# Optimization experiments

Hardware: AMD Instinct MI355X
Metric: run time of the kernel (lower is better)

Reference implementation:

```python
import math
import jax, jax.numpy as jnp
import numpy as np


def _proj(x, w, b):
    # 1x1x1 Conv3d == pointwise channel matmul: (B,C,T,H,W) x (O,C) -> (B,O,T,H,W)
    return jnp.einsum('bcthw,oc->bothw', x, w) + b[None, :, None, None, None]


def setup_inputs() -> dict:
    key = jax.random.key(0)
    ks = jax.random.split(key, 16)
    B, C, T, H, W = 2, 64, 16, 14, 14
    CI = C // 2
    s_in = 1.0 / math.sqrt(C)
    s_out = 1.0 / math.sqrt(CI)
    inp = {'x': jax.random.normal(ks[0], (B, C, T, H, W), jnp.float32)}
    # QKV projections for spatial (s) and temporal (t) branches: (CI, C) weights
    pnames = ['qs', 'ks', 'vs', 'qt', 'kt', 'vt']
    for i, n in enumerate(pnames):
        inp['W' + n] = jax.random.normal(ks[1 + i], (CI, C), jnp.float32) * s_in
        inp['b' + n] = jax.random.normal(ks[7 + i], (CI,), jnp.float32) * 0.01
    # output projection W: (C, CI)
    inp['Ww'] = jax.random.normal(ks[13], (C, CI), jnp.float32) * s_out
    inp['bw'] = jax.random.normal(ks[14], (C,), jnp.float32) * 0.01
    return inp


def reference(x, Wqs, bqs, Wks, bks, Wvs, bvs, Wqt, bqt, Wkt, bkt, Wvt, bvt, Ww, bw):
    B, C, T, H, W = x.shape
    CI = Wqs.shape[0]
    N = CI * H * W  # flat dim after original's raw .view (mixes channel & spatial/time)
    scale = 1.0 / math.sqrt(T)

    # ---- spatial branch: .view(B, T, -1) raw reshape of (B,CI,T,H,W) ----
    qs = _proj(x, Wqs, bqs).reshape(B, T, N).transpose(0, 2, 1)   # (B,N,T)
    ks_ = _proj(x, Wks, bks).reshape(B, T, N)                     # (B,T,N)
    vs = _proj(x, Wvs, bvs).reshape(B, T, N).transpose(0, 2, 1)   # (B,N,T)
    attn_s = jax.nn.softmax(jnp.einsum('bnt,btm->bnm', qs, ks_) * scale, axis=-1)  # (B,N,N)
    ys = jnp.einsum('bnm,bmt->bnt', attn_s, vs)                   # (B,N,T)
    ys = ys.transpose(0, 2, 1).reshape(B, CI, T, H, W)

    # ---- temporal branch: .view(B, CI*H*W, -1) raw reshape ----
    qt = _proj(x, Wqt, bqt).reshape(B, N, T).transpose(0, 2, 1)   # (B,T,N)
    kt = _proj(x, Wkt, bkt).reshape(B, N, T)                      # (B,N,T)
    vt = _proj(x, Wvt, bvt).reshape(B, N, T).transpose(0, 2, 1)   # (B,T,N)
    attn_t = jax.nn.softmax(jnp.einsum('btn,bns->bts', qt, kt) * scale, axis=-1)  # (B,T,T)
    yt = jnp.einsum('bts,bsn->btn', attn_t, vt)                   # (B,T,N)
    yt = yt.transpose(0, 2, 1).reshape(B, CI, T, H, W)

    y = ys + yt
    return _proj(y, Ww, bw) + x
```

## Files before the change

kernel.cpp:

```cpp
#include <hip/hip_runtime.h>
#include <math.h>

#define S3   3136
#define PB   100352
#define XB   200704
#define NN   6272

typedef __attribute__((ext_vector_type(8))) short bf16x8;
typedef __attribute__((ext_vector_type(4))) float f32x4;

__device__ inline ushort f2bf(float f) {
    uint u = __float_as_uint(f);
    return (ushort)((u + 0x7FFFu + ((u >> 16) & 1u)) >> 16);
}

__global__ __launch_bounds__(256) void proj_kernel(
    const float* __restrict__ x,
    const float* __restrict__ W0, const float* __restrict__ b0,
    const float* __restrict__ W1, const float* __restrict__ b1,
    const float* __restrict__ W2, const float* __restrict__ b2,
    const float* __restrict__ W3, const float* __restrict__ b3,
    const float* __restrict__ W4, const float* __restrict__ b4,
    const float* __restrict__ W5, const float* __restrict__ b5,
    ushort* __restrict__ Qb, ushort* __restrict__ Kb, ushort* __restrict__ Vb,
    float* __restrict__ Qt, float* __restrict__ Kt, float* __restrict__ Vt,
    int* __restrict__ cnt)
{
    if (blockIdx.x == 0 && blockIdx.y == 0 && blockIdx.z == 0 && threadIdx.x < 2)
        cnt[threadIdx.x] = 0;

    const float* Wp; const float* bp;
    switch (blockIdx.y) {
        case 0:  Wp = W0; bp = b0; break;
        case 1:  Wp = W1; bp = b1; break;
        case 2:  Wp = W2; bp = b2; break;
        case 3:  Wp = W3; bp = b3; break;
        case 4:  Wp = W4; bp = b4; break;
        default: Wp = W5; bp = b5; break;
    }
    int z = blockIdx.z;

    int gid = blockIdx.x * 256 + threadIdx.x;
    if (gid >= 2 * S3) return;
    int b = (gid >= S3) ? 1 : 0;
    int s = gid - b * S3;

    float xr[64];
    #pragma unroll
    for (int c = 0; c < 64; ++c) xr[c] = x[(size_t)b * XB + (size_t)c * S3 + s];

    float a[16];
    #pragma unroll
    for (int oo = 0; oo < 16; ++oo) {
        int o = z * 16 + oo;
        float acc = bp[o];
        #pragma unroll
        for (int c = 0; c < 64; ++c) acc = fmaf(Wp[o * 64 + c], xr[c], acc);
        a[oo] = acc;
    }

    if (blockIdx.y < 2) {
        const float sc = (blockIdx.y == 0) ? 0.36067376022224085f : 1.0f;
        ushort* ob = (blockIdx.y == 0) ? Qb : Kb;
        #pragma unroll
        for (int h = 0; h < 2; ++h) {
            int n = h * S3 + s;
            uint u0 = f2bf(a[0 + h] * sc)  | ((uint)f2bf(a[2 + h]  * sc) << 16);
            uint u1 = f2bf(a[4 + h] * sc)  | ((uint)f2bf(a[6 + h]  * sc) << 16);
            uint u2 = f2bf(a[8 + h] * sc)  | ((uint)f2bf(a[10 + h] * sc) << 16);
            uint u3 = f2bf(a[12 + h] * sc) | ((uint)f2bf(a[14 + h] * sc) << 16);
            *(uint4*)(ob + ((size_t)(b * NN + n) * 16 + z * 8)) = make_uint4(u0, u1, u2, u3);
        }
    } else if (blockIdx.y == 2) {
        #pragma unroll
        for (int oo = 0; oo < 16; ++oo) {
            int o = z * 16 + oo;
            Vb[(size_t)(b * 16 + (o >> 1)) * NN + (o & 1) * S3 + s] = f2bf(a[oo]);
        }
    } else {
        float* op = (blockIdx.y == 3) ? Qt : (blockIdx.y == 4) ? Kt : Vt;
        #pragma unroll
        for (int oo = 0; oo < 16; ++oo)
            op[(size_t)b * PB + (size_t)(z * 16 + oo) * S3 + s] = a[oo];
    }
}

__global__ __launch_bounds__(256, 4) void attn_kernel(
    const ushort* __restrict__ Qb, const ushort* __restrict__ Kb,
    const ushort* __restrict__ Vb, const float* __restrict__ Qt,
    const float* __restrict__ Kt,
    float* __restrict__ Y, float* __restrict__ Gpart,
    float* __restrict__ At, int* __restrict__ cnt)
{
    __shared__ __align__(16) char smem[16384];
    const int tid = threadIdx.x;
    const int bid = blockIdx.x;

    if (bid < 784) {
        ushort* ptile = (ushort*)smem;
        float*  smY   = (float*)(smem + 5120);
        float*  sml   = (float*)(smem + 9472);

        int wave = __builtin_amdgcn_readfirstlane((int)(tid >> 6));
        int lane = tid & 63;
        int col  = lane & 15;
        int kg   = lane >> 4;
        int b    = (bid >= 392) ? 1 : 0;
        int ntile = bid - b * 392;
        int nbase = ntile * 16;
        int m0    = wave * 1568;

        bf16x8 qf = {0, 0, 0, 0, 0, 0, 0, 0};
        if (kg < 2)
            qf = *(const bf16x8*)(Qb + ((size_t)(b * NN + nbase + col) * 16 + kg * 8));

        const bf16x8 ones = {16256, 16256, 16256, 16256, 16256, 16256, 16256, 16256};
        f32x4 zero4 = {0.f, 0.f, 0.f, 0.f};
        f32x4 yacc  = zero4;
        f32x4 lacc  = zero4;

        ushort* myt = ptile + wave * 640;

        for (int it = 0; it < 49; ++it) {
            int mb = m0 + it * 32;
            bf16x8 vf = *(const bf16x8*)(Vb + ((size_t)(b * 16 + col) * NN + mb + kg * 8));

            #pragma unroll
            for (int tile = 0; tile < 2; ++tile) {
                int mt = mb + tile * 16;
                bf16x8 kf = {0, 0, 0, 0, 0, 0, 0, 0};
                if (kg < 2)
                    kf = *(const bf16x8*)(Kb + ((size_t)(b * NN + mt + col) * 16 + kg * 8));
                f32x4 st = __builtin_amdgcn_mfma_f32_16x16x32_bf16(kf, qf, zero4, 0, 0, 0);
                float p0 = __builtin_amdgcn_exp2f(st[0]);
                float p1 = __builtin_amdgcn_exp2f(st[1]);
                float p2 = __builtin_amdgcn_exp2f(st[2]);
                float p3 = __builtin_amdgcn_exp2f(st[3]);
                uint lo = f2bf(p0) | ((uint)f2bf(p1) << 16);
                uint hi = f2bf(p2) | ((uint)f2bf(p3) << 16);
                *(uint2*)(myt + (col * 40 + tile * 16 + kg * 4)) = make_uint2(lo, hi);
            }
            bf16x8 pf = *(bf16x8*)(myt + (col * 40 + kg * 8));
            yacc = __builtin_amdgcn_mfma_f32_16x16x32_bf16(vf, pf, yacc, 0, 0, 0);
            lacc = __builtin_amdgcn_mfma_f32_16x16x32_bf16(ones, pf, lacc, 0, 0, 0);
        }

        #pragma unroll
        for (int r = 0; r < 4; ++r)
            smY[(wave * 16 + kg * 4 + r) * 17 + col] = yacc[r];
        if (kg == 0) sml[wave * 16 + col] = lacc[0];
        __syncthreads();

        int t  = tid >> 4;
        int nn = tid & 15;
        float a = smY[(0 * 16 + t) * 17 + nn] + smY[(1 * 16 + t) * 17 + nn]
                + smY[(2 * 16 + t) * 17 + nn] + smY[(3 * 16 + t) * 17 + nn];
        float l = sml[0 * 16 + nn] + sml[1 * 16 + nn]
                + sml[2 * 16 + nn] + sml[3 * 16 + nn];
        Y[(size_t)b * PB + (size_t)t * NN + nbase + nn] = a / l;
    } else {
        float* qs = (float*)smem;
        float* ks = qs + 1568;
        int*   flag = (int*)(smem + 16000);

        int gb = bid - 784;
        int b  = gb >> 4;
        int ch = gb & 15;
        int t  = tid >> 4, s2 = tid & 15;

        float acc = 0.0f;
        for (int sub = 0; sub < 4; ++sub) {
            size_t base = (size_t)b * PB + (size_t)(ch * 392 + sub * 98) * 16;
            __syncthreads();
            for (int i = tid; i < 392; i += 256) {
                ((float4*)qs)[i] = ((const float4*)(Qt + base))[i];
                ((float4*)ks)[i] = ((const float4*)(Kt + base))[i];
            }
            __syncthreads();
            #pragma unroll 7
            for (int n = 0; n < 98; ++n)
                acc = fmaf(qs[n * 16 + t], ks[n * 16 + s2], acc);
        }
        Gpart[(size_t)(b * 16 + ch) * 256 + tid] = acc;

        __threadfence();
        __syncthreads();
        if (tid == 0) {
            int old = atomicAdd(cnt + b, 1);
            *flag = (old == 15);
        }
        __syncthreads();
        if (*flag) {
            __threadfence();
            float a = 0.0f;
            #pragma unroll
            for (int c = 0; c < 16; ++c)
                a += Gpart[(size_t)(b * 16 + c) * 256 + tid];
            qs[tid] = a * 0.25f;
            __syncthreads();
            if (tid < 16) {
                const float* Lr = &qs[tid * 16];
                float mx = -1e30f;
                #pragma unroll
                for (int s = 0; s < 16; ++s) mx = fmaxf(mx, Lr[s]);
                float e[16]; float sm = 0.0f;
                #pragma unroll
                for (int s = 0; s < 16; ++s) { e[s] = __expf(Lr[s] - mx); sm += e[s]; }
                float inv = 1.0f / sm;
                #pragma unroll
                for (int s = 0; s < 16; ++s) At[b * 256 + tid * 16 + s] = e[s] * inv;
            }
        }
    }
}

__global__ __launch_bounds__(256) void merge_final(
    const float* __restrict__ Y, const float* __restrict__ At,
    const float* __restrict__ Vt, const float* __restrict__ x,
    const float* __restrict__ Ww, const float* __restrict__ bw,
    float* __restrict__ out)
{
    __shared__ float Ash[16 * 17];
    __shared__ float Wsh[64 * 36];
    __shared__ float Ysh[16 * 36];

    int b  = blockIdx.y;
    int sc = blockIdx.x;
    int tid = threadIdx.x;

    {
        int s2 = tid >> 4, t2 = tid & 15;
        Ash[s2 * 17 + t2] = At[b * 256 + t2 * 16 + s2];
        for (int i = tid; i < 2048; i += 256)
            Wsh[(i >> 5) * 36 + (i & 31)] = Ww[i];
    }
    __syncthreads();

    #pragma unroll
    for (int k = 0; k < 2; ++k) {
        int idx = tid + k * 256;
        int ss = idx & 15;
        int ci = idx >> 4;
        int s  = sc * 16 + ss;
        int t  = ci >> 1;
        int nn = (ci & 1) * S3 + s;

        float ys = Y[(size_t)b * PB + (size_t)ci * S3 + s];

        int t2 = nn & 15;
        const float4* vp = (const float4*)(Vt + (size_t)b * PB + (size_t)t * NN + (nn & ~15));
        float4 v0 = vp[0], v1 = vp[1], v2 = vp[2], v3 = vp[3];
        float yt = Ash[0 * 17 + t2] * v0.x;
        yt = fmaf(Ash[1 * 17 + t2],  v0.y, yt); yt = fmaf(Ash[2 * 17 + t2],  v0.z, yt);
        yt = fmaf(Ash[3 * 17 + t2],  v0.w, yt); yt = fmaf(Ash[4 * 17 + t2],  v1.x, yt);
        yt = fmaf(Ash[5 * 17 + t2],  v1.y, yt); yt = fmaf(Ash[6 * 17 + t2],  v1.z, yt);
        yt = fmaf(Ash[7 * 17 + t2],  v1.w, yt); yt = fmaf(Ash[8 * 17 + t2],  v2.x, yt);
        yt = fmaf(Ash[9 * 17 + t2],  v2.y, yt); yt = fmaf(Ash[10 * 17 + t2], v2.z, yt);
        yt = fmaf(Ash[11 * 17 + t2], v2.w, yt); yt = fmaf(Ash[12 * 17 + t2], v3.x, yt);
        yt = fmaf(Ash[13 * 17 + t2], v3.y, yt); yt = fmaf(Ash[14 * 17 + t2], v3.z, yt);
        yt = fmaf(Ash[15 * 17 + t2], v3.w, yt);

        Ysh[ss * 36 + ci] = ys + yt;
    }
    __syncthreads();

    int ss  = tid & 15;
    int cg4 = tid >> 4;
    int s   = sc * 16 + ss;

    float acc[4];
    #pragma unroll
    for (int k = 0; k < 4; ++k) acc[k] = bw[k * 16 + cg4];

    #pragma unroll
    for (int cb = 0; cb < 32; cb += 4) {
        float4 y4 = *(const float4*)&Ysh[ss * 36 + cb];
        #pragma unroll
        for (int k = 0; k < 4; ++k) {
            float4 w4 = *(const float4*)&Wsh[(k * 16 + cg4) * 36 + cb];
            acc[k] = fmaf(w4.x, y4.x, acc[k]);
            acc[k] = fmaf(w4.y, y4.y, acc[k]);
            acc[k] = fmaf(w4.z, y4.z, acc[k]);
            acc[k] = fmaf(w4.w, y4.w, acc[k]);
        }
    }

    #pragma unroll
    for (int k = 0; k < 4; ++k) {
        int c = k * 16 + cg4;
        size_t o = (size_t)b * XB + (size_t)c * S3 + s;
        out[o] = x[o] + acc[k];
    }
}

extern "C" void kernel_launch(void* const* d_in, const int* in_sizes, int n_in,
                              void* d_out, int out_size, void* d_ws, size_t ws_size,
                              hipStream_t stream)
{
    const float* x   = (const float*)d_in[0];
    const float* Wqs = (const float*)d_in[1];  const float* bqs = (const float*)d_in[2];
    const float* Wks = (const float*)d_in[3];  const float* bks = (const float*)d_in[4];
    const float* Wvs = (const float*)d_in[5];  const float* bvs = (const float*)d_in[6];
    const float* Wqt = (const float*)d_in[7];  const float* bqt = (const float*)d_in[8];
    const float* Wkt = (const float*)d_in[9];  const float* bkt = (const float*)d_in[10];
    const float* Wvt = (const float*)d_in[11]; const float* bvt = (const float*)d_in[12];
    const float* Ww  = (const float*)d_in[13]; const float* bw  = (const float*)d_in[14];

    float* ws = (float*)d_ws;
    int*    cnt = (int*)ws;
    ushort* Qb  = (ushort*)(ws + 4);
    ushort* Kb  = (ushort*)(ws + 100356);
    ushort* Vb  = (ushort*)(ws + 200708);
    float* Qt   = ws + 301060;
    float* Kt   = ws + 501764;
    float* Vt   = ws + 702468;
    float* Y    = ws + 903172;
    float* Gpart = ws + 1103876;
    float* At    = ws + 1112068;

    proj_kernel<<<dim3(25, 6, 2), 256, 0, stream>>>(
        x, Wqs, bqs, Wks, bks, Wvs, bvs, Wqt, bqt, Wkt, bkt, Wvt, bvt,
        Qb, Kb, Vb, Qt, Kt, Vt, cnt);

    attn_kernel<<<816, 256, 0, stream>>>(Qb, Kb, Vb, Qt, Kt, Y, Gpart, At, cnt);

    merge_final<<<dim3(196, 2), 256, 0, stream>>>(
        Y, At, Vt, x, Ww, bw, (float*)d_out);
}
```

Baseline: 149.8 us.

## Split spatial attention key range across eight waves with double-buffered P tiles

The attention kernel goes from 256 to 512 threads, so each of 8 waves handles 784 keys instead of 4 waves handling 1568. The per-wave P scratch is double-buffered and a tail block covers the leftover 16 keys. The float-to-bf16 conversion of exp values now truncates instead of rounding. The aim is more parallelism per tile and a shorter serial loop. The cost is a larger LDS footprint, an 8-way reduction, and idle threads in the temporal-Gram blocks.

```diff
diff --git a/kernel.cpp b/kernel.cpp
--- a/kernel.cpp
+++ b/kernel.cpp
@@ -85,21 +85,21 @@
     }
 }
 
-__global__ __launch_bounds__(256, 4) void attn_kernel(
+__global__ __launch_bounds__(512, 4) void attn_kernel(
     const ushort* __restrict__ Qb, const ushort* __restrict__ Kb,
     const ushort* __restrict__ Vb, const float* __restrict__ Qt,
     const float* __restrict__ Kt,
     float* __restrict__ Y, float* __restrict__ Gpart,
     float* __restrict__ At, int* __restrict__ cnt)
 {
-    __shared__ __align__(16) char smem[16384];
+    __shared__ __align__(16) char smem[30208];
     const int tid = threadIdx.x;
     const int bid = blockIdx.x;
 
     if (bid < 784) {
         ushort* ptile = (ushort*)smem;
-        float*  smY   = (float*)(smem + 5120);
-        float*  sml   = (float*)(smem + 9472);
+        float*  smY   = (float*)(smem + 20480);
+        float*  sml   = (float*)(smem + 29184);
 
         int wave = __builtin_amdgcn_readfirstlane((int)(tid >> 6));
         int lane = tid & 63;
@@ -108,7 +108,7 @@
         int b    = (bid >= 392) ? 1 : 0;
         int ntile = bid - b * 392;
         int nbase = ntile * 16;
-        int m0    = wave * 1568;
+        int m0    = wave * 784;
 
         bf16x8 qf = {0, 0, 0, 0, 0, 0, 0, 0};
         if (kg < 2)
@@ -119,28 +119,55 @@
         f32x4 yacc  = zero4;
         f32x4 lacc  = zero4;
 
-        ushort* myt = ptile + wave * 640;
-
-        for (int it = 0; it < 49; ++it) {
+        ushort* myt = ptile + wave * 1280;
+
+        const ushort* Vrow = Vb + ((size_t)(b * 16 + col) * NN);
+        const ushort* Krow = Kb + ((size_t)b * NN) * 16;
+
+        #pragma unroll 2
+        for (int it = 0; it < 24; ++it) {
+            ushort* buf = myt + (it & 1) * 640;
             int mb = m0 + it * 32;
-            bf16x8 vf = *(const bf16x8*)(Vb + ((size_t)(b * 16 + col) * NN + mb + kg * 8));
+            bf16x8 vf = *(const bf16x8*)(Vrow + mb + kg * 8);
 
             #pragma unroll
             for (int tile = 0; tile < 2; ++tile) {
                 int mt = mb + tile * 16;
                 bf16x8 kf = {0, 0, 0, 0, 0, 0, 0, 0};
                 if (kg < 2)
-                    kf = *(const bf16x8*)(Kb + ((size_t)(b * NN + mt + col) * 16 + kg * 8));
+                    kf = *(const bf16x8*)(Krow + (size_t)(mt + col) * 16 + kg * 8);
                 f32x4 st = __builtin_amdgcn_mfma_f32_16x16x32_bf16(kf, qf, zero4, 0, 0, 0);
                 float p0 = __builtin_amdgcn_exp2f(st[0]);
                 float p1 = __builtin_amdgcn_exp2f(st[1]);
                 float p2 = __builtin_amdgcn_exp2f(st[2]);
                 float p3 = __builtin_amdgcn_exp2f(st[3]);
-                uint lo = f2bf(p0) | ((uint)f2bf(p1) << 16);
-                uint hi = f2bf(p2) | ((uint)f2bf(p3) << 16);
-                *(uint2*)(myt + (col * 40 + tile * 16 + kg * 4)) = make_uint2(lo, hi);
-            }
-            bf16x8 pf = *(bf16x8*)(myt + (col * 40 + kg * 8));
+                uint lo = (__float_as_uint(p0) >> 16) | (__float_as_uint(p1) & 0xFFFF0000u);
+                uint hi = (__float_as_uint(p2) >> 16) | (__float_as_uint(p3) & 0xFFFF0000u);
+                *(uint2*)(buf + (col * 40 + tile * 16 + kg * 4)) = make_uint2(lo, hi);
+            }
+            bf16x8 pf = *(bf16x8*)(buf + (col * 40 + kg * 8));
+            yacc = __builtin_amdgcn_mfma_f32_16x16x32_bf16(vf, pf, yacc, 0, 0, 0);
+            lacc = __builtin_amdgcn_mfma_f32_16x16x32_bf16(ones, pf, lacc, 0, 0, 0);
+        }
+
+        {
+            int mb = m0 + 768;
+            bf16x8 vf = {0, 0, 0, 0, 0, 0, 0, 0};
+            bf16x8 kf = {0, 0, 0, 0, 0, 0, 0, 0};
+            if (kg < 2) {
+                vf = *(const bf16x8*)(Vrow + mb + kg * 8);
+                kf = *(const bf16x8*)(Krow + (size_t)(mb + col) * 16 + kg * 8);
+            }
+            f32x4 st = __builtin_amdgcn_mfma_f32_16x16x32_bf16(kf, qf, zero4, 0, 0, 0);
+            float p0 = __builtin_amdgcn_exp2f(st[0]);
+            float p1 = __builtin_amdgcn_exp2f(st[1]);
+            float p2 = __builtin_amdgcn_exp2f(st[2]);
+            float p3 = __builtin_amdgcn_exp2f(st[3]);
+            uint lo = (__float_as_uint(p0) >> 16) | (__float_as_uint(p1) & 0xFFFF0000u);
+            uint hi = (__float_as_uint(p2) >> 16) | (__float_as_uint(p3) & 0xFFFF0000u);
+            *(uint2*)(myt + (col * 40 + kg * 4)) = make_uint2(lo, hi);
+            bf16x8 pf = {0, 0, 0, 0, 0, 0, 0, 0};
+            if (kg < 2) pf = *(bf16x8*)(myt + (col * 40 + kg * 8));
             yacc = __builtin_amdgcn_mfma_f32_16x16x32_bf16(vf, pf, yacc, 0, 0, 0);
             lacc = __builtin_amdgcn_mfma_f32_16x16x32_bf16(ones, pf, lacc, 0, 0, 0);
         }
@@ -151,17 +178,21 @@
         if (kg == 0) sml[wave * 16 + col] = lacc[0];
         __syncthreads();
 
-        int t  = tid >> 4;
-        int nn = tid & 15;
-        float a = smY[(0 * 16 + t) * 17 + nn] + smY[(1 * 16 + t) * 17 + nn]
-                + smY[(2 * 16 + t) * 17 + nn] + smY[(3 * 16 + t) * 17 + nn];
-        float l = sml[0 * 16 + nn] + sml[1 * 16 + nn]
-                + sml[2 * 16 + nn] + sml[3 * 16 + nn];
-        Y[(size_t)b * PB + (size_t)t * NN + nbase + nn] = a / l;
+        if (tid < 256) {
+            int t  = tid >> 4;
+            int nn = tid & 15;
+            float a = 0.0f, l = 0.0f;
+            #pragma unroll
+            for (int w = 0; w < 8; ++w) {
+                a += smY[(w * 16 + t) * 17 + nn];
+                l += sml[w * 16 + nn];
+            }
+            Y[(size_t)b * PB + (size_t)t * NN + nbase + nn] = a / l;
+        }
     } else {
         float* qs = (float*)smem;
         float* ks = qs + 1568;
-        int*   flag = (int*)(smem + 16000);
+        int*   flag = (int*)(smem + 30000);
 
         int gb = bid - 784;
         int b  = gb >> 4;
@@ -172,16 +203,19 @@
         for (int sub = 0; sub < 4; ++sub) {
             size_t base = (size_t)b * PB + (size_t)(ch * 392 + sub * 98) * 16;
             __syncthreads();
-            for (int i = tid; i < 392; i += 256) {
+            for (int i = tid; i < 392; i += 512) {
                 ((float4*)qs)[i] = ((const float4*)(Qt + base))[i];
                 ((float4*)ks)[i] = ((const float4*)(Kt + base))[i];
             }
             __syncthreads();
-            #pragma unroll 7
-            for (int n = 0; n < 98; ++n)
-                acc = fmaf(qs[n * 16 + t], ks[n * 16 + s2], acc);
-        }
-        Gpart[(size_t)(b * 16 + ch) * 256 + tid] = acc;
+            if (tid < 256) {
+                #pragma unroll 7
+                for (int n = 0; n < 98; ++n)
+                    acc = fmaf(qs[n * 16 + t], ks[n * 16 + s2], acc);
+            }
+        }
+        if (tid < 256)
+            Gpart[(size_t)(b * 16 + ch) * 256 + tid] = acc;
 
         __threadfence();
         __syncthreads();
@@ -192,11 +226,13 @@
         __syncthreads();
         if (*flag) {
             __threadfence();
-            float a = 0.0f;
-            #pragma unroll
-            for (int c = 0; c < 16; ++c)
-                a += Gpart[(size_t)(b * 16 + c) * 256 + tid];
-            qs[tid] = a * 0.25f;
+            if (tid < 256) {
+                float a = 0.0f;
+                #pragma unroll
+                for (int c = 0; c < 16; ++c)
+                    a += Gpart[(size_t)(b * 16 + c) * 256 + tid];
+                qs[tid] = a * 0.25f;
+            }
             __syncthreads();
             if (tid < 16) {
                 const float* Lr = &qs[tid * 16];
@@ -322,7 +358,7 @@
         x, Wqs, bqs, Wks, bks, Wvs, bvs, Wqt, bqt, Wkt, bkt, Wvt, bvt,
         Qb, Kb, Vb, Qt, Kt, Vt, cnt);
 
-    attn_kernel<<<816, 256, 0, stream>>>(Qb, Kb, Vb, Qt, Kt, Y, Gpart, At, cnt);
+    attn_kernel<<<816, 512, 0, stream>>>(Qb, Kb, Vb, Qt, Kt, Y, Gpart, At, cnt);
 
     merge_final<<<dim3(196, 2), 256, 0, stream>>>(
         Y, At, Vt, x, Ww, bw, (float*)d_out);
```

After: 149.1 us. About the same (-0.5%).

## Batch spatial attention loop into 128-key groups and truncate bf16 packing

Applied to the files above, without the earlier changes.

The spatial attention inner loop now handles four 32-key chunks per iteration. It issues all V and K global loads up front, then runs eight score MFMAs with exp2, and stores the probabilities into four per-wave LDS tiles before the PV MFMAs. A tail step covers the remaining 32 keys. This is meant to expose more memory-level parallelism and cut loop overhead. The round-to-nearest bf16 conversion is also replaced with plain truncation, which saves ALU work but slightly changes numerics. Shared memory per block grows from 16 KB to 25 KB, which may limit occupancy, and register pressure rises.

```diff
diff --git a/kernel.cpp b/kernel.cpp
--- a/kernel.cpp
+++ b/kernel.cpp
@@ -92,14 +92,14 @@
     float* __restrict__ Y, float* __restrict__ Gpart,
     float* __restrict__ At, int* __restrict__ cnt)
 {
-    __shared__ __align__(16) char smem[16384];
+    __shared__ __align__(16) char smem[25600];
     const int tid = threadIdx.x;
     const int bid = blockIdx.x;
 
     if (bid < 784) {
         ushort* ptile = (ushort*)smem;
-        float*  smY   = (float*)(smem + 5120);
-        float*  sml   = (float*)(smem + 9472);
+        float*  smY   = (float*)(smem + 20480);
+        float*  sml   = (float*)(smem + 24832);
 
         int wave = __builtin_amdgcn_readfirstlane((int)(tid >> 6));
         int lane = tid & 63;
@@ -119,25 +119,64 @@
         f32x4 yacc  = zero4;
         f32x4 lacc  = zero4;
 
-        ushort* myt = ptile + wave * 640;
-
-        for (int it = 0; it < 49; ++it) {
-            int mb = m0 + it * 32;
-            bf16x8 vf = *(const bf16x8*)(Vb + ((size_t)(b * 16 + col) * NN + mb + kg * 8));
-
-            #pragma unroll
-            for (int tile = 0; tile < 2; ++tile) {
-                int mt = mb + tile * 16;
-                bf16x8 kf = {0, 0, 0, 0, 0, 0, 0, 0};
+        ushort* myt = ptile + wave * 2560;
+
+        const ushort* Vrow = Vb + ((size_t)(b * 16 + col) * NN);
+        const ushort* Krow = Kb + ((size_t)b * NN) * 16;
+
+        for (int g = 0; g < 12; ++g) {
+            int mb0 = m0 + g * 128;
+
+            bf16x8 vf[4];
+            #pragma unroll
+            for (int i = 0; i < 4; ++i)
+                vf[i] = *(const bf16x8*)(Vrow + mb0 + i * 32 + kg * 8);
+            bf16x8 kf[8];
+            #pragma unroll
+            for (int i = 0; i < 8; ++i) {
+                bf16x8 kz = {0, 0, 0, 0, 0, 0, 0, 0};
                 if (kg < 2)
-                    kf = *(const bf16x8*)(Kb + ((size_t)(b * NN + mt + col) * 16 + kg * 8));
-                f32x4 st = __builtin_amdgcn_mfma_f32_16x16x32_bf16(kf, qf, zero4, 0, 0, 0);
+                    kz = *(const bf16x8*)(Krow + (size_t)(mb0 + i * 16 + col) * 16 + kg * 8);
+                kf[i] = kz;
+            }
+
+            #pragma unroll
+            for (int i = 0; i < 8; ++i) {
+                f32x4 st = __builtin_amdgcn_mfma_f32_16x16x32_bf16(kf[i], qf, zero4, 0, 0, 0);
                 float p0 = __builtin_amdgcn_exp2f(st[0]);
                 float p1 = __builtin_amdgcn_exp2f(st[1]);
                 float p2 = __builtin_amdgcn_exp2f(st[2]);
                 float p3 = __builtin_amdgcn_exp2f(st[3]);
-                uint lo = f2bf(p0) | ((uint)f2bf(p1) << 16);
-                uint hi = f2bf(p2) | ((uint)f2bf(p3) << 16);
+                uint lo = (__float_as_uint(p0) >> 16) | (__float_as_uint(p1) & 0xFFFF0000u);
+                uint hi = (__float_as_uint(p2) >> 16) | (__float_as_uint(p3) & 0xFFFF0000u);
+                ushort* buf = myt + (i >> 1) * 640;
+                *(uint2*)(buf + (col * 40 + (i & 1) * 16 + kg * 4)) = make_uint2(lo, hi);
+            }
+
+            #pragma unroll
+            for (int i = 0; i < 4; ++i) {
+                bf16x8 pf = *(bf16x8*)(myt + i * 640 + (col * 40 + kg * 8));
+                yacc = __builtin_amdgcn_mfma_f32_16x16x32_bf16(vf[i], pf, yacc, 0, 0, 0);
+                lacc = __builtin_amdgcn_mfma_f32_16x16x32_bf16(ones, pf, lacc, 0, 0, 0);
+            }
+        }
+
+        {
+            int mb = m0 + 1536;
+            bf16x8 vf = *(const bf16x8*)(Vrow + mb + kg * 8);
+            #pragma unroll
+            for (int tile = 0; tile < 2; ++tile) {
+                int mt = mb + tile * 16;
+                bf16x8 kz = {0, 0, 0, 0, 0, 0, 0, 0};
+                if (kg < 2)
+                    kz = *(const bf16x8*)(Krow + (size_t)(mt + col) * 16 + kg * 8);
+                f32x4 st = __builtin_amdgcn_mfma_f32_16x16x32_bf16(kz, qf, zero4, 0, 0, 0);
+                float p0 = __builtin_amdgcn_exp2f(st[0]);
+                float p1 = __builtin_amdgcn_exp2f(st[1]);
+                float p2 = __builtin_amdgcn_exp2f(st[2]);
+                float p3 = __builtin_amdgcn_exp2f(st[3]);
+                uint lo = (__float_as_uint(p0) >> 16) | (__float_as_uint(p1) & 0xFFFF0000u);
+                uint hi = (__float_as_uint(p2) >> 16) | (__float_as_uint(p3) & 0xFFFF0000u);
                 *(uint2*)(myt + (col * 40 + tile * 16 + kg * 4)) = make_uint2(lo, hi);
             }
             bf16x8 pf = *(bf16x8*)(myt + (col * 40 + kg * 8));
@@ -161,7 +200,7 @@
     } else {
         float* qs = (float*)smem;
         float* ks = qs + 1568;
-        int*   flag = (int*)(smem + 16000);
+        int*   flag = (int*)(smem + 25344);
 
         int gb = bid - 784;
         int b  = gb >> 4;
```

Result: faster. 144.9 us (-3.3%).
